# Kernel optimization log

Hardware: AMD Instinct MI355X
Metric: run time of the kernel (lower is better)

## Reference

```python
import jax, jax.numpy as jnp
import numpy as np

N, E, G = 20000, 320000, 64
IN, ED, H, F, FC, NC = 6, 2, 4, 64, 64, 2
HF = H * F


def _glorot(key, shape):
    fan_in, fan_out = shape[0], shape[-1]
    s = jnp.sqrt(6.0 / (fan_in + fan_out))
    return jax.random.uniform(key, shape, jnp.float32, -s, s)


def setup_inputs() -> dict:
    key = jax.random.key(0)
    ks = jax.random.split(key, 24)
    inp = {
        "x": jax.random.normal(ks[0], (N, IN), jnp.float32),
        "edge_index": jax.random.randint(ks[1], (2, E), 0, N, jnp.int64),
        "edge_attr": jax.random.normal(ks[2], (E, ED), jnp.float32),
        "batch": jnp.sort(jax.random.randint(ks[3], (N,), 0, G, jnp.int64)),
        # layer 0 (GATv2, in=6 -> 4 heads x 64)
        "Wl0": _glorot(ks[4], (IN, HF)), "bl0": jnp.zeros((HF,), jnp.float32),
        "Wr0": _glorot(ks[5], (IN, HF)), "br0": jnp.zeros((HF,), jnp.float32),
        "We0": _glorot(ks[6], (ED, HF)),
        "att0": _glorot(ks[7], (H, F)), "b0": jnp.zeros((HF,), jnp.float32),
        "proj0": _glorot(ks[8], (IN, HF)),  # residual projection 6 -> 256
        # layer 1 (GATv2, in=256 -> 4 heads x 64); residual is identity (256==256)
        "Wl1": _glorot(ks[9], (HF, HF)), "bl1": jnp.zeros((HF,), jnp.float32),
        "Wr1": _glorot(ks[10], (HF, HF)), "br1": jnp.zeros((HF,), jnp.float32),
        "We1": _glorot(ks[11], (ED, HF)),
        "att1": _glorot(ks[12], (H, F)), "b1": jnp.zeros((HF,), jnp.float32),
        # head
        "Wp": _glorot(ks[13], (HF, FC)), "bp": jnp.zeros((FC,), jnp.float32),
        "Wc": _glorot(ks[14], (FC, NC)), "bc": jnp.zeros((NC,), jnp.float32),
    }
    return inp


def _add_self_loops_mean(src, dst, eattr):
    # PyG add_self_loops(fill_value='mean'): self-loop attr = mean of incoming edge_attr
    s = jax.ops.segment_sum(eattr, dst, num_segments=N)
    c = jax.ops.segment_sum(jnp.ones((eattr.shape[0], 1), eattr.dtype), dst, num_segments=N)
    loop_attr = s / jnp.maximum(c, 1.0)
    idx = jnp.arange(N, dtype=src.dtype)
    return (jnp.concatenate([src, idx]), jnp.concatenate([dst, idx]),
            jnp.concatenate([eattr, loop_attr], axis=0))


def _gatv2(x, src, dst, ee, Wl, bl, Wr, br, att, bias):
    # ee: precomputed edge projection [E2, H, F]
    xl = (x @ Wl + bl).reshape(N, H, F)   # source transform
    xr = (x @ Wr + br).reshape(N, H, F)   # target transform
    m = jax.nn.leaky_relu(xl[src] + xr[dst] + ee, 0.2)   # [E2, H, F]
    logits = jnp.einsum('ehf,hf->eh', m, att)            # [E2, H]
    mx = jax.ops.segment_max(logits, dst, num_segments=N)
    ex = jnp.exp(logits - mx[dst])
    den = jax.ops.segment_sum(ex, dst, num_segments=N)
    alpha = ex / den[dst]                                 # scatter-softmax over dst
    out = jax.ops.segment_sum(xl[src] * alpha[:, :, None], dst, num_segments=N)
    return out.reshape(N, HF) + bias


def reference(x, edge_index, edge_attr, batch,
              Wl0, bl0, Wr0, br0, We0, att0, b0, proj0,
              Wl1, bl1, Wr1, br1, We1, att1, b1,
              Wp, bp, Wc, bc):
    src, dst, eattr = _add_self_loops_mean(edge_index[0], edge_index[1], edge_attr)
    # layer 0 (residual: projected input); dropout is a no-op in eval mode
    h = _gatv2(x, src, dst, (eattr @ We0).reshape(-1, H, F), Wl0, bl0, Wr0, br0, att0, b0)
    x1 = jax.nn.elu(h) + x @ proj0
    # layer 1 (residual: identity)
    h = _gatv2(x1, src, dst, (eattr @ We1).reshape(-1, H, F), Wl1, bl1, Wr1, br1, att1, b1)
    x2 = jax.nn.elu(h) + x1
    # pre-pool MLP + global mean pool over graphs + classifier
    z = jax.nn.elu(x2 @ Wp + bp)                           # [N, FC]
    gs = jax.ops.segment_sum(z, batch, num_segments=G)
    gc = jax.ops.segment_sum(jnp.ones((N, 1), z.dtype), batch, num_segments=G)
    pooled = gs / jnp.maximum(gc, 1.0)                     # [G, FC]
    return pooled @ Wc + bc                                # [G, NC]
```

## Files before the change

kernel.cpp:

```cpp
#include <hip/hip_runtime.h>
#include <math.h>

#define NN   20000
#define NE   320000
#define NG   64
#define INF_ 6
#define EDF  2
#define NH   4
#define FD   64
#define HF   256
#define FCD  64
#define NCD  2
#define CAP  64

#define ZB   ((NN + 255) / 256)
#define WCB  512
#define L0B  ((NN + 3) / 4)

typedef short bf16x8 __attribute__((ext_vector_type(8)));
typedef float f32x4  __attribute__((ext_vector_type(4)));

static __device__ __forceinline__ unsigned short f2bf(float f) {
  unsigned u = __float_as_uint(f);
  unsigned r = 0x7fffu + ((u >> 16) & 1u);
  return (unsigned short)((u + r) >> 16);
}
static __device__ __forceinline__ float4 bf2f4(uint2 p) {
  float4 v;
  v.x = __uint_as_float(p.x << 16);
  v.y = __uint_as_float(p.x & 0xffff0000u);
  v.z = __uint_as_float(p.y << 16);
  v.w = __uint_as_float(p.y & 0xffff0000u);
  return v;
}


__global__ __launch_bounds__(256) void k_init(
    int* __restrict__ cnt, float* __restrict__ gpool,
    const float* __restrict__ Wl1, const float* __restrict__ Wr1,
    unsigned short* __restrict__ Wsw,
    const float* __restrict__ x,
    const float* __restrict__ Wl0, const float* __restrict__ bl0,
    const float* __restrict__ Wr0, const float* __restrict__ br0,
    unsigned short* __restrict__ xlb, float* __restrict__ xr) {
  int b = blockIdx.x;
  int t = threadIdx.x;
  if (b < ZB) {
    int i = b * 256 + t;
    if (i < NN) cnt[i] = 0;
  } else if (b == ZB) {
    for (int i = t; i < NG * FCD; i += 256) gpool[i] = 0.f;
  } else if (b < ZB + 1 + WCB) {
    int id = (b - ZB - 1) * 256 + t;
    int j = id & 7, lane = (id >> 3) & 63, kk8 = (id >> 9) & 7, ntg = id >> 12;
    int n = ntg * 16 + (lane & 15);
    int k = kk8 * 32 + (lane >> 4) * 8 + j;
    float v = (n < 256) ? Wl1[k * 256 + n] : Wr1[k * 256 + (n - 256)];
    Wsw[id] = f2bf(v);
  } else {
    int w = t >> 6, lane = t & 63;
    int n = (b - ZB - 1 - WCB) * 4 + w;
    if (n >= NN) return;
    int cb = lane << 2;
    float4 al = *(const float4*)&bl0[cb];
    float4 ar = *(const float4*)&br0[cb];
#pragma unroll
    for (int k = 0; k < INF_; ++k) {
      float xv = x[n * INF_ + k];
      float4 wl = *(const float4*)&Wl0[k * HF + cb];
      float4 wr = *(const float4*)&Wr0[k * HF + cb];
      al.x = fmaf(xv, wl.x, al.x); al.y = fmaf(xv, wl.y, al.y);
      al.z = fmaf(xv, wl.z, al.z); al.w = fmaf(xv, wl.w, al.w);
      ar.x = fmaf(xv, wr.x, ar.x); ar.y = fmaf(xv, wr.y, ar.y);
      ar.z = fmaf(xv, wr.z, ar.z); ar.w = fmaf(xv, wr.w, ar.w);
    }
    uint2 pk;
    pk.x = (unsigned)f2bf(al.x) | ((unsigned)f2bf(al.y) << 16);
    pk.y = (unsigned)f2bf(al.z) | ((unsigned)f2bf(al.w) << 16);
    *(uint2*)&xlb[(size_t)n * HF + cb] = pk;
    *(float4*)&xr[(size_t)n * HF + cb] = ar;
  }
}


__global__ void k_scatter(const int* __restrict__ ei, const float* __restrict__ ea,
                          int* __restrict__ cnt, uint2* __restrict__ rec) {
  int i = blockIdx.x * blockDim.x + threadIdx.x;
  if (i >= NE) return;
  int s = ei[i], d = ei[NE + i];
  float2 a = *(const float2*)&ea[2 * i];
  int pos = atomicAdd(&cnt[d], 1);
  if (pos < CAP)
    rec[(size_t)d * CAP + pos] = make_uint2((unsigned)(s * 512),
                                            (unsigned)f2bf(a.x) | ((unsigned)f2bf(a.y) << 16));
}


__global__ __launch_bounds__(256) void k_l1_mfma(
    const unsigned short* __restrict__ x1b,
    const unsigned short* __restrict__ Wsw,
    const float* __restrict__ bl, const float* __restrict__ br,
    unsigned short* __restrict__ xlb, float* __restrict__ xr) {
  __shared__ float so[64][132];
  int t = threadIdx.x;
  int row0 = blockIdx.x * 64;
  int w = t >> 6, lane = t & 63;
  int quad = lane >> 4, ln = lane & 15;
  int y = blockIdx.y;

  int arow = row0 + w * 16 + ln; if (arow >= NN) arow = NN - 1;
  const unsigned short* aptr = x1b + (size_t)arow * HF + quad * 8;

  f32x4 acc[8];
#pragma unroll
  for (int i = 0; i < 8; ++i) acc[i] = (f32x4){0.f, 0.f, 0.f, 0.f};

  for (int kk8 = 0; kk8 < 8; ++kk8) {
    bf16x8 af = *(const bf16x8*)(aptr + kk8 * 32);
#pragma unroll
    for (int nt = 0; nt < 8; ++nt) {
      bf16x8 bfr = *(const bf16x8*)&Wsw[(size_t)((((y * 8 + nt) * 8 + kk8) * 64) + lane) * 8];
      acc[nt] = __builtin_amdgcn_mfma_f32_16x16x32_bf16(af, bfr, acc[nt], 0, 0, 0);
    }
  }
#pragma unroll
  for (int nt = 0; nt < 8; ++nt)
#pragma unroll
    for (int rg = 0; rg < 4; ++rg)
      so[w * 16 + quad * 4 + rg][nt * 16 + ln] = acc[nt][rg];
  __syncthreads();

  if (y < 2) {
    int cb8 = (t & 15) * 8;
    int rsub = t >> 4;
    int gcol = y * 128 + cb8;
    float4 b0 = *(const float4*)&bl[gcol];
    float4 b1 = *(const float4*)&bl[gcol + 4];
#pragma unroll
    for (int i = 0; i < 4; ++i) {
      int row = i * 16 + rsub;
      int grow = row0 + row;
      if (grow < NN) {
        unsigned h0 = f2bf(so[row][cb8 + 0] + b0.x);
        unsigned h1 = f2bf(so[row][cb8 + 1] + b0.y);
        unsigned h2 = f2bf(so[row][cb8 + 2] + b0.z);
        unsigned h3 = f2bf(so[row][cb8 + 3] + b0.w);
        unsigned h4 = f2bf(so[row][cb8 + 4] + b1.x);
        unsigned h5 = f2bf(so[row][cb8 + 5] + b1.y);
        unsigned h6 = f2bf(so[row][cb8 + 6] + b1.z);
        unsigned h7 = f2bf(so[row][cb8 + 7] + b1.w);
        uint4 pk;
        pk.x = h0 | (h1 << 16);
        pk.y = h2 | (h3 << 16);
        pk.z = h4 | (h5 << 16);
        pk.w = h6 | (h7 << 16);
        *(uint4*)&xlb[(size_t)grow * HF + gcol] = pk;
      }
    }
  } else {
    int cb4 = (t & 31) * 4;
    int rsub = t >> 5;
    int gcol = (y - 2) * 128 + cb4;
    float4 b4 = *(const float4*)&br[gcol];
#pragma unroll
    for (int i = 0; i < 8; ++i) {
      int row = i * 8 + rsub;
      int grow = row0 + row;
      if (grow < NN) {
        float4 v;
        v.x = so[row][cb4 + 0] + b4.x;
        v.y = so[row][cb4 + 1] + b4.y;
        v.z = so[row][cb4 + 2] + b4.z;
        v.w = so[row][cb4 + 3] + b4.w;
        *(float4*)&xr[(size_t)grow * HF + gcol] = v;
      }
    }
  }
}


template <bool L0>
__global__ __launch_bounds__(256) void k_agg(
    const unsigned short* __restrict__ xlb, const float* xr_,
    const int* __restrict__ cnt, const uint2* __restrict__ rec,
    const float* __restrict__ att, const float* __restrict__ We,
    const float* __restrict__ bias,
    const float* __restrict__ x, const float* __restrict__ proj0,
    unsigned short* __restrict__ x1bout,
    const unsigned short* __restrict__ x1bin, float* x2out) {
  int wid = (blockIdx.x * 256 + threadIdx.x) >> 6;
  if (wid >= NN) return;
  int lane = threadIdx.x & 63;
  int n = wid;
  int cb = lane << 2;

  float4 xr4 = *(const float4*)&xr_[(size_t)n * HF + cb];
  float4 at4 = *(const float4*)&att[cb];
  float4 w04 = *(const float4*)&We[cb];
  float4 w14 = *(const float4*)&We[HF + cb];

  int nreal = min(cnt[n], CAP);
  const uint2* recn = rec + (size_t)n * CAP;
  const char* xlbase = (const char*)xlb + (size_t)(cb * 2);

  float a0s = 0.f, a1s = 0.f;
  for (int e = lane; e < nreal; e += 64) {
    uint2 r = recn[e];
    a0s += __uint_as_float(r.y << 16);
    a1s += __uint_as_float(r.y & 0xffff0000u);
  }
#pragma unroll
  for (int o = 32; o; o >>= 1) {
    a0s += __shfl_xor(a0s, o, 64);
    a1s += __shfl_xor(a1s, o, 64);
  }
  float im = 1.0f / fmaxf((float)nreal, 1.0f);
  float a0m = a0s * im, a1m = a1s * im;

  uint2 ps = *(const uint2*)(xlbase + (unsigned)(n * 512));
  float4 vS = bf2f4(ps);
  float tS;
  {
    float4 mm;
    mm.x = vS.x + fmaf(a0m, w04.x, fmaf(a1m, w14.x, xr4.x));
    mm.y = vS.y + fmaf(a0m, w04.y, fmaf(a1m, w14.y, xr4.y));
    mm.z = vS.z + fmaf(a0m, w04.z, fmaf(a1m, w14.z, xr4.z));
    mm.w = vS.w + fmaf(a0m, w04.w, fmaf(a1m, w14.w, xr4.w));
    mm.x = fmaxf(mm.x, 0.2f * mm.x);
    mm.y = fmaxf(mm.y, 0.2f * mm.y);
    mm.z = fmaxf(mm.z, 0.2f * mm.z);
    mm.w = fmaxf(mm.w, 0.2f * mm.w);
    float tt = mm.x * at4.x;
    tt = fmaf(mm.y, at4.y, tt);
    tt = fmaf(mm.z, at4.z, tt);
    tt = fmaf(mm.w, at4.w, tt);
    tt += __shfl_xor(tt, 1, 64);
    tt += __shfl_xor(tt, 2, 64);
    tt += __shfl_xor(tt, 4, 64);
    tt += __shfl_xor(tt, 8, 64);
    tS = tt;
  }
  float den = 1.f;
  float4 acc = vS;

  if (nreal > 0) {
    int lastE = nreal - 1;
    for (int e0 = 0; e0 < nreal; e0 += 4) {
      uint2 r4[4], p4[4];
#pragma unroll
      for (int i = 0; i < 4; ++i)
        r4[i] = recn[min(e0 + i, lastE)];
#pragma unroll
      for (int i = 0; i < 4; ++i)
        p4[i] = *(const uint2*)(xlbase + r4[i].x);

      float t4[4];
#pragma unroll
      for (int i = 0; i < 4; ++i) {
        float4 vC = bf2f4(p4[i]);
        float a0 = __uint_as_float(r4[i].y << 16);
        float a1 = __uint_as_float(r4[i].y & 0xffff0000u);
        float4 mm;
        mm.x = vC.x + fmaf(a0, w04.x, fmaf(a1, w14.x, xr4.x));
        mm.y = vC.y + fmaf(a0, w04.y, fmaf(a1, w14.y, xr4.y));
        mm.z = vC.z + fmaf(a0, w04.z, fmaf(a1, w14.z, xr4.z));
        mm.w = vC.w + fmaf(a0, w04.w, fmaf(a1, w14.w, xr4.w));
        mm.x = fmaxf(mm.x, 0.2f * mm.x);
        mm.y = fmaxf(mm.y, 0.2f * mm.y);
        mm.z = fmaxf(mm.z, 0.2f * mm.z);
        mm.w = fmaxf(mm.w, 0.2f * mm.w);
        float tt = mm.x * at4.x;
        tt = fmaf(mm.y, at4.y, tt);
        tt = fmaf(mm.z, at4.z, tt);
        tt = fmaf(mm.w, at4.w, tt);
        t4[i] = tt;
      }
#pragma unroll
      for (int o = 1; o <= 8; o <<= 1) {
#pragma unroll
        for (int i = 0; i < 4; ++i) t4[i] += __shfl_xor(t4[i], o, 64);
      }
#pragma unroll
      for (int i = 0; i < 4; ++i) {
        float w = (e0 + i <= lastE) ? __expf(fminf(t4[i] - tS, 80.f)) : 0.f;
        float4 vC = bf2f4(p4[i]);
        den += w;
        acc.x = fmaf(w, vC.x, acc.x);
        acc.y = fmaf(w, vC.y, acc.y);
        acc.z = fmaf(w, vC.z, acc.z);
        acc.w = fmaf(w, vC.w, acc.w);
      }
    }
  }

  float inv = 1.0f / den;
  float4 b4 = *(const float4*)&bias[cb];
  float4 o;
  o.x = fmaf(acc.x, inv, b4.x);
  o.y = fmaf(acc.y, inv, b4.y);
  o.z = fmaf(acc.z, inv, b4.z);
  o.w = fmaf(acc.w, inv, b4.w);
  o.x = (o.x > 0.f) ? o.x : expm1f(o.x);
  o.y = (o.y > 0.f) ? o.y : expm1f(o.y);
  o.z = (o.z > 0.f) ? o.z : expm1f(o.z);
  o.w = (o.w > 0.f) ? o.w : expm1f(o.w);

  if (L0) {
    float4 rr = make_float4(0.f, 0.f, 0.f, 0.f);
#pragma unroll
    for (int k = 0; k < INF_; ++k) {
      float xv = x[n * INF_ + k];
      float4 p = *(const float4*)&proj0[k * HF + cb];
      rr.x = fmaf(xv, p.x, rr.x);
      rr.y = fmaf(xv, p.y, rr.y);
      rr.z = fmaf(xv, p.z, rr.z);
      rr.w = fmaf(xv, p.w, rr.w);
    }
    o.x += rr.x; o.y += rr.y; o.z += rr.z; o.w += rr.w;
    uint2 pk;
    pk.x = (unsigned)f2bf(o.x) | ((unsigned)f2bf(o.y) << 16);
    pk.y = (unsigned)f2bf(o.z) | ((unsigned)f2bf(o.w) << 16);
    *(uint2*)&x1bout[(size_t)n * HF + cb] = pk;
  } else {
    float4 x1v = bf2f4(*(const uint2*)&x1bin[(size_t)n * HF + cb]);
    o.x += x1v.x; o.y += x1v.y; o.z += x1v.z; o.w += x1v.w;
    *(float4*)&x2out[(size_t)n * HF + cb] = o;
  }
}


__global__ __launch_bounds__(256) void k_pool(
    const float* __restrict__ x2, const float* __restrict__ Wp,
    const float* __restrict__ bp, const int* __restrict__ batch,
    float* __restrict__ gpool) {
  __shared__ float xs[32 * HF];
  __shared__ int gid_s[32];
  int t = threadIdx.x;
  int row0 = blockIdx.x * 32;
  const float4* s4 = (const float4*)(x2 + (size_t)row0 * HF);
  float4* d4 = (float4*)xs;
#pragma unroll
  for (int i = 0; i < 8; ++i) d4[i * 256 + t] = s4[i * 256 + t];
  if (t < 32) gid_s[t] = batch[row0 + t];
  __syncthreads();
  int j = t & 63, rg = t >> 6;
  float acc[8];
#pragma unroll
  for (int rr = 0; rr < 8; ++rr) acc[rr] = 0.f;
  for (int k4 = 0; k4 < HF / 4; ++k4) {
    float w0 = Wp[(k4 * 4 + 0) * FCD + j];
    float w1 = Wp[(k4 * 4 + 1) * FCD + j];
    float w2 = Wp[(k4 * 4 + 2) * FCD + j];
    float w3 = Wp[(k4 * 4 + 3) * FCD + j];
#pragma unroll
    for (int rr = 0; rr < 8; ++rr) {
      float4 xv = *(const float4*)&xs[(rg * 8 + rr) * HF + k4 * 4];
      acc[rr] = fmaf(xv.x, w0, acc[rr]);
      acc[rr] = fmaf(xv.y, w1, acc[rr]);
      acc[rr] = fmaf(xv.z, w2, acc[rr]);
      acc[rr] = fmaf(xv.w, w3, acc[rr]);
    }
  }
  float b = bp[j];
  int gprev = gid_s[rg * 8];
  float run = 0.f;
#pragma unroll
  for (int rr = 0; rr < 8; ++rr) {
    float a = acc[rr] + b;
    float z = (a > 0.f) ? a : expm1f(a);
    int g = gid_s[rg * 8 + rr];
    if (g != gprev) {
      atomicAdd(&gpool[gprev * FCD + j], run);
      run = 0.f; gprev = g;
    }
    run += z;
  }
  atomicAdd(&gpool[gprev * FCD + j], run);
}


__global__ void k_head(const float* __restrict__ gpool, const int* __restrict__ batch,
                       const float* __restrict__ Wc, const float* __restrict__ bc,
                       float* __restrict__ out) {
  int t = threadIdx.x;
  int g = t >> 1, k = t & 1;
  int lo = 0, hi = NN;
  while (lo < hi) { int mid = (lo + hi) >> 1; if (batch[mid] < g) lo = mid + 1; else hi = mid; }
  int c0 = lo;
  lo = 0; hi = NN;
  while (lo < hi) { int mid = (lo + hi) >> 1; if (batch[mid] < g + 1) lo = mid + 1; else hi = mid; }
  int c1 = lo;
  float inv = 1.0f / fmaxf((float)(c1 - c0), 1.0f);
  float a = bc[k];
  for (int j = 0; j < FCD; ++j)
    a = fmaf(gpool[g * FCD + j] * inv, Wc[j * NCD + k], a);
  out[g * NCD + k] = a;
}


extern "C" void kernel_launch(void* const* d_in, const int* in_sizes, int n_in,
                              void* d_out, int out_size, void* d_ws, size_t ws_size,
                              hipStream_t stream) {
  const float* x    = (const float*)d_in[0];
  const int*   ei   = (const int*)d_in[1];
  const float* ea   = (const float*)d_in[2];
  const int*   batch= (const int*)d_in[3];
  const float* Wl0  = (const float*)d_in[4];
  const float* bl0  = (const float*)d_in[5];
  const float* Wr0  = (const float*)d_in[6];
  const float* br0  = (const float*)d_in[7];
  const float* We0  = (const float*)d_in[8];
  const float* att0 = (const float*)d_in[9];
  const float* b0   = (const float*)d_in[10];
  const float* proj0= (const float*)d_in[11];
  const float* Wl1  = (const float*)d_in[12];
  const float* bl1  = (const float*)d_in[13];
  const float* Wr1  = (const float*)d_in[14];
  const float* br1  = (const float*)d_in[15];
  const float* We1  = (const float*)d_in[16];
  const float* att1 = (const float*)d_in[17];
  const float* b1   = (const float*)d_in[18];
  const float* Wp   = (const float*)d_in[19];
  const float* bp   = (const float*)d_in[20];
  const float* Wc   = (const float*)d_in[21];
  const float* bc   = (const float*)d_in[22];
  float* out = (float*)d_out;

  char* ws = (char*)d_ws;
  size_t off = 0;
  int*   cnt    = (int*)(ws + off);   off += (NN * 4 + 15) / 16 * 16;
  uint2* rec    = (uint2*)(ws + off); off += (size_t)NN * CAP * 8;
  unsigned short* xlb = (unsigned short*)(ws + off); off += (size_t)NN * HF * 2;
  float* xr     = (float*)(ws + off); off += (size_t)NN * HF * 4;
  unsigned short* x1b = (unsigned short*)(ws + off); off += (size_t)NN * HF * 2;
  float* gpool  = (float*)(ws + off); off += NG * FCD * 4;
  unsigned short* Wsw = (unsigned short*)(ws + off); off += 512 * 256 * 2;
  float* x2     = xr;
  (void)ws_size; (void)in_sizes; (void)n_in; (void)out_size;

  k_init<<<ZB + 1 + WCB + L0B, 256, 0, stream>>>(
      cnt, gpool, Wl1, Wr1, Wsw, x, Wl0, bl0, Wr0, br0, xlb, xr);

  k_scatter<<<(NE + 255) / 256, 256, 0, stream>>>(ei, ea, cnt, rec);

  k_agg<true><<<(NN * 64 + 255) / 256, 256, 0, stream>>>(
      xlb, xr, cnt, rec, att0, We0, b0, x, proj0, x1b, nullptr, nullptr);

  k_l1_mfma<<<dim3((NN + 63) / 64, 4), 256, 0, stream>>>(x1b, Wsw, bl1, br1, xlb, xr);
  k_agg<false><<<(NN * 64 + 255) / 256, 256, 0, stream>>>(
      xlb, xr, cnt, rec, att1, We1, b1, nullptr, nullptr, nullptr, x1b, x2);

  k_pool<<<NN / 32, 256, 0, stream>>>(x2, Wp, bp, batch, gpool);
  k_head<<<1, 128, 0, stream>>>(gpool, batch, Wc, bc, out);
}
```

Baseline: 269.4 us.

## Store xr and x2 intermediates in bf16 and widen layer-1 GEMM tiles

```diff
diff --git a/kernel.cpp b/kernel.cpp
--- a/kernel.cpp
+++ b/kernel.cpp
@@ -42,7 +42,7 @@
     const float* __restrict__ x,
     const float* __restrict__ Wl0, const float* __restrict__ bl0,
     const float* __restrict__ Wr0, const float* __restrict__ br0,
-    unsigned short* __restrict__ xlb, float* __restrict__ xr) {
+    unsigned short* __restrict__ xlb, unsigned short* __restrict__ xrb) {
   int b = blockIdx.x;
   int t = threadIdx.x;
   if (b < ZB) {
@@ -78,7 +78,10 @@
     pk.x = (unsigned)f2bf(al.x) | ((unsigned)f2bf(al.y) << 16);
     pk.y = (unsigned)f2bf(al.z) | ((unsigned)f2bf(al.w) << 16);
     *(uint2*)&xlb[(size_t)n * HF + cb] = pk;
-    *(float4*)&xr[(size_t)n * HF + cb] = ar;
+    uint2 pr;
+    pr.x = (unsigned)f2bf(ar.x) | ((unsigned)f2bf(ar.y) << 16);
+    pr.y = (unsigned)f2bf(ar.z) | ((unsigned)f2bf(ar.w) << 16);
+    *(uint2*)&xrb[(size_t)n * HF + cb] = pr;
   }
 }
 
@@ -100,101 +103,66 @@
     const unsigned short* __restrict__ x1b,
     const unsigned short* __restrict__ Wsw,
     const float* __restrict__ bl, const float* __restrict__ br,
-    unsigned short* __restrict__ xlb, float* __restrict__ xr) {
-  __shared__ float so[64][132];
+    unsigned short* __restrict__ xlb, unsigned short* __restrict__ xrb) {
+  __shared__ unsigned short so[64][264];
   int t = threadIdx.x;
   int row0 = blockIdx.x * 64;
   int w = t >> 6, lane = t & 63;
   int quad = lane >> 4, ln = lane & 15;
   int y = blockIdx.y;
+  const float* bias = y ? br : bl;
+  unsigned short* dst = y ? xrb : xlb;
 
   int arow = row0 + w * 16 + ln; if (arow >= NN) arow = NN - 1;
   const unsigned short* aptr = x1b + (size_t)arow * HF + quad * 8;
 
-  f32x4 acc[8];
-#pragma unroll
-  for (int i = 0; i < 8; ++i) acc[i] = (f32x4){0.f, 0.f, 0.f, 0.f};
+  f32x4 acc[16];
+#pragma unroll
+  for (int i = 0; i < 16; ++i) acc[i] = (f32x4){0.f, 0.f, 0.f, 0.f};
 
   for (int kk8 = 0; kk8 < 8; ++kk8) {
     bf16x8 af = *(const bf16x8*)(aptr + kk8 * 32);
 #pragma unroll
-    for (int nt = 0; nt < 8; ++nt) {
-      bf16x8 bfr = *(const bf16x8*)&Wsw[(size_t)((((y * 8 + nt) * 8 + kk8) * 64) + lane) * 8];
+    for (int nt = 0; nt < 16; ++nt) {
+      bf16x8 bfr = *(const bf16x8*)&Wsw[(size_t)((((y * 16 + nt) * 8 + kk8) * 64) + lane) * 8];
       acc[nt] = __builtin_amdgcn_mfma_f32_16x16x32_bf16(af, bfr, acc[nt], 0, 0, 0);
     }
   }
 #pragma unroll
-  for (int nt = 0; nt < 8; ++nt)
+  for (int nt = 0; nt < 16; ++nt) {
+    float bv = bias[nt * 16 + ln];
 #pragma unroll
     for (int rg = 0; rg < 4; ++rg)
-      so[w * 16 + quad * 4 + rg][nt * 16 + ln] = acc[nt][rg];
+      so[w * 16 + quad * 4 + rg][nt * 16 + ln] = f2bf(acc[nt][rg] + bv);
+  }
   __syncthreads();
-
-  if (y < 2) {
-    int cb8 = (t & 15) * 8;
-    int rsub = t >> 4;
-    int gcol = y * 128 + cb8;
-    float4 b0 = *(const float4*)&bl[gcol];
-    float4 b1 = *(const float4*)&bl[gcol + 4];
-#pragma unroll
-    for (int i = 0; i < 4; ++i) {
-      int row = i * 16 + rsub;
-      int grow = row0 + row;
-      if (grow < NN) {
-        unsigned h0 = f2bf(so[row][cb8 + 0] + b0.x);
-        unsigned h1 = f2bf(so[row][cb8 + 1] + b0.y);
-        unsigned h2 = f2bf(so[row][cb8 + 2] + b0.z);
-        unsigned h3 = f2bf(so[row][cb8 + 3] + b0.w);
-        unsigned h4 = f2bf(so[row][cb8 + 4] + b1.x);
-        unsigned h5 = f2bf(so[row][cb8 + 5] + b1.y);
-        unsigned h6 = f2bf(so[row][cb8 + 6] + b1.z);
-        unsigned h7 = f2bf(so[row][cb8 + 7] + b1.w);
-        uint4 pk;
-        pk.x = h0 | (h1 << 16);
-        pk.y = h2 | (h3 << 16);
-        pk.z = h4 | (h5 << 16);
-        pk.w = h6 | (h7 << 16);
-        *(uint4*)&xlb[(size_t)grow * HF + gcol] = pk;
-      }
-    }
-  } else {
-    int cb4 = (t & 31) * 4;
-    int rsub = t >> 5;
-    int gcol = (y - 2) * 128 + cb4;
-    float4 b4 = *(const float4*)&br[gcol];
-#pragma unroll
-    for (int i = 0; i < 8; ++i) {
-      int row = i * 8 + rsub;
-      int grow = row0 + row;
-      if (grow < NN) {
-        float4 v;
-        v.x = so[row][cb4 + 0] + b4.x;
-        v.y = so[row][cb4 + 1] + b4.y;
-        v.z = so[row][cb4 + 2] + b4.z;
-        v.w = so[row][cb4 + 3] + b4.w;
-        *(float4*)&xr[(size_t)grow * HF + gcol] = v;
-      }
-    }
+#pragma unroll
+  for (int i = 0; i < 8; ++i) {
+    int idx = i * 256 + t;
+    int row = idx >> 5, c8 = idx & 31;
+    int grow = row0 + row;
+    if (grow < NN)
+      *(uint4*)&dst[(size_t)grow * HF + c8 * 8] = *(const uint4*)&so[row][c8 * 8];
   }
 }
 
 
 template <bool L0>
 __global__ __launch_bounds__(256) void k_agg(
-    const unsigned short* __restrict__ xlb, const float* xr_,
+    const unsigned short* __restrict__ xlb, const unsigned short* xrb_,
     const int* __restrict__ cnt, const uint2* __restrict__ rec,
     const float* __restrict__ att, const float* __restrict__ We,
     const float* __restrict__ bias,
     const float* __restrict__ x, const float* __restrict__ proj0,
     unsigned short* __restrict__ x1bout,
-    const unsigned short* __restrict__ x1bin, float* x2out) {
+    const unsigned short* __restrict__ x1bin, unsigned short* x2bout) {
   int wid = (blockIdx.x * 256 + threadIdx.x) >> 6;
   if (wid >= NN) return;
   int lane = threadIdx.x & 63;
   int n = wid;
   int cb = lane << 2;
 
-  float4 xr4 = *(const float4*)&xr_[(size_t)n * HF + cb];
+  float4 xr4 = bf2f4(*(const uint2*)&xrb_[(size_t)n * HF + cb]);
   float4 at4 = *(const float4*)&att[cb];
   float4 w04 = *(const float4*)&We[cb];
   float4 w14 = *(const float4*)&We[HF + cb];
@@ -324,23 +292,33 @@
   } else {
     float4 x1v = bf2f4(*(const uint2*)&x1bin[(size_t)n * HF + cb]);
     o.x += x1v.x; o.y += x1v.y; o.z += x1v.z; o.w += x1v.w;
-    *(float4*)&x2out[(size_t)n * HF + cb] = o;
+    uint2 pk;
+    pk.x = (unsigned)f2bf(o.x) | ((unsigned)f2bf(o.y) << 16);
+    pk.y = (unsigned)f2bf(o.z) | ((unsigned)f2bf(o.w) << 16);
+    *(uint2*)&x2bout[(size_t)n * HF + cb] = pk;
   }
 }
 
 
 __global__ __launch_bounds__(256) void k_pool(
-    const float* __restrict__ x2, const float* __restrict__ Wp,
+    const unsigned short* __restrict__ x2b, const float* __restrict__ Wp,
     const float* __restrict__ bp, const int* __restrict__ batch,
     float* __restrict__ gpool) {
   __shared__ float xs[32 * HF];
   __shared__ int gid_s[32];
   int t = threadIdx.x;
   int row0 = blockIdx.x * 32;
-  const float4* s4 = (const float4*)(x2 + (size_t)row0 * HF);
-  float4* d4 = (float4*)xs;
-#pragma unroll
-  for (int i = 0; i < 8; ++i) d4[i * 256 + t] = s4[i * 256 + t];
+  const uint4* s4 = (const uint4*)(x2b + (size_t)row0 * HF);
+#pragma unroll
+  for (int i = 0; i < 4; ++i) {
+    int idx = i * 256 + t;
+    uint4 p = s4[idx];
+    int base = idx * 8;
+    float4 lo = bf2f4(make_uint2(p.x, p.y));
+    float4 hi = bf2f4(make_uint2(p.z, p.w));
+    *(float4*)&xs[base] = lo;
+    *(float4*)&xs[base + 4] = hi;
+  }
   if (t < 32) gid_s[t] = batch[row0 + t];
   __syncthreads();
   int j = t & 63, rg = t >> 6;
@@ -431,25 +409,25 @@
   int*   cnt    = (int*)(ws + off);   off += (NN * 4 + 15) / 16 * 16;
   uint2* rec    = (uint2*)(ws + off); off += (size_t)NN * CAP * 8;
   unsigned short* xlb = (unsigned short*)(ws + off); off += (size_t)NN * HF * 2;
-  float* xr     = (float*)(ws + off); off += (size_t)NN * HF * 4;
+  unsigned short* xrb = (unsigned short*)(ws + off); off += (size_t)NN * HF * 2;
   unsigned short* x1b = (unsigned short*)(ws + off); off += (size_t)NN * HF * 2;
   float* gpool  = (float*)(ws + off); off += NG * FCD * 4;
   unsigned short* Wsw = (unsigned short*)(ws + off); off += 512 * 256 * 2;
-  float* x2     = xr;
+  unsigned short* x2b = xrb;
   (void)ws_size; (void)in_sizes; (void)n_in; (void)out_size;
 
   k_init<<<ZB + 1 + WCB + L0B, 256, 0, stream>>>(
-      cnt, gpool, Wl1, Wr1, Wsw, x, Wl0, bl0, Wr0, br0, xlb, xr);
+      cnt, gpool, Wl1, Wr1, Wsw, x, Wl0, bl0, Wr0, br0, xlb, xrb);
 
   k_scatter<<<(NE + 255) / 256, 256, 0, stream>>>(ei, ea, cnt, rec);
 
   k_agg<true><<<(NN * 64 + 255) / 256, 256, 0, stream>>>(
-      xlb, xr, cnt, rec, att0, We0, b0, x, proj0, x1b, nullptr, nullptr);
-
-  k_l1_mfma<<<dim3((NN + 63) / 64, 4), 256, 0, stream>>>(x1b, Wsw, bl1, br1, xlb, xr);
+      xlb, xrb, cnt, rec, att0, We0, b0, x, proj0, x1b, nullptr, nullptr);
+
+  k_l1_mfma<<<dim3((NN + 63) / 64, 2), 256, 0, stream>>>(x1b, Wsw, bl1, br1, xlb, xrb);
   k_agg<false><<<(NN * 64 + 255) / 256, 256, 0, stream>>>(
-      xlb, xr, cnt, rec, att1, We1, b1, nullptr, nullptr, nullptr, x1b, x2);
-
-  k_pool<<<NN / 32, 256, 0, stream>>>(x2, Wp, bp, batch, gpool);
+      xlb, xrb, cnt, rec, att1, We1, b1, nullptr, nullptr, nullptr, x1b, x2b);
+
+  k_pool<<<NN / 32, 256, 0, stream>>>(x2b, Wp, bp, batch, gpool);
   k_head<<<1, 128, 0, stream>>>(gpool, batch, Wc, bc, out);
 }
```

After: 261.8 us (median of 2 runs). 2.8% less time.
